# Kernel optimization log

Hardware: AMD Instinct MI355X
Metric: run time of the kernel (lower is better)

The kernel has to match this reference:

```python
import jax, jax.numpy as jnp
import numpy as np

DIM = 512
EXPAND = 2
D_INNER = DIM * EXPAND            # 1024
HEADDIM = DIM * EXPAND // 8       # 128
NHEADS = D_INNER // HEADDIM       # 8
D_STATE = 128
D_CONV = 4
CONV_DIM = D_INNER + 2 * D_STATE  # 1280 (x, B, C channels)
D_IN_PROJ = 2 * D_INNER + 2 * D_STATE + NHEADS  # 2312
BSZ = 4
IMG = (16, 16, 16)                # 4096 tokens


def setup_inputs() -> dict:
    key = jax.random.key(0)
    ks = jax.random.split(key, 8)
    x = jax.random.normal(ks[0], (BSZ, DIM, *IMG), jnp.float32)
    in_proj_w = jax.random.normal(ks[1], (D_IN_PROJ, DIM), jnp.float32) * (DIM ** -0.5)
    conv_w = jax.random.normal(ks[2], (CONV_DIM, D_CONV), jnp.float32) * 0.3
    conv_b = jax.random.normal(ks[3], (CONV_DIM,), jnp.float32) * 0.1
    dt_bias = jax.random.normal(ks[4], (NHEADS,), jnp.float32) * 0.5
    A_log = jnp.log(jnp.arange(1, NHEADS + 1, dtype=jnp.float32))
    D_param = jnp.ones((NHEADS,), jnp.float32) + 0.1 * jax.random.normal(ks[5], (NHEADS,), jnp.float32)
    norm_w = jnp.ones((D_INNER,), jnp.float32)
    out_proj_w = jax.random.normal(ks[6], (DIM, D_INNER), jnp.float32) * (D_INNER ** -0.5)
    return dict(x=x, in_proj_w=in_proj_w, conv_w=conv_w, conv_b=conv_b,
                dt_bias=dt_bias, A_log=A_log, D_param=D_param,
                norm_w=norm_w, out_proj_w=out_proj_w)


def reference(x, in_proj_w, conv_w, conv_b, dt_bias, A_log, D_param, norm_w, out_proj_w):
    Bsz, C = x.shape[:2]
    img_dims = x.shape[2:]
    u = x.reshape(Bsz, C, -1).transpose(0, 2, 1)          # [b, L, d_model]
    L = u.shape[1]

    zxbcdt = jnp.einsum('bld,ed->ble', u, in_proj_w)      # [b, L, 2312]
    z = zxbcdt[..., :D_INNER]                             # gate
    xBC = zxbcdt[..., D_INNER:D_INNER + CONV_DIM]
    dt = zxbcdt[..., D_INNER + CONV_DIM:]                 # [b, L, h]
    dt = jax.nn.softplus(dt + dt_bias)

    # causal depthwise conv1d (kernel 4) + SiLU
    xp = jnp.pad(xBC, ((0, 0), (D_CONV - 1, 0), (0, 0)))
    conv = conv_b + sum(xp[:, k:k + L, :] * conv_w[:, k] for k in range(D_CONV))
    xBC = jax.nn.silu(conv)

    xs = xBC[..., :D_INNER].reshape(Bsz, L, NHEADS, HEADDIM)   # [b, L, h, p]
    Bmat = xBC[..., D_INNER:D_INNER + D_STATE]                 # [b, L, n] (ngroups=1)
    Cmat = xBC[..., D_INNER + D_STATE:]                        # [b, L, n]

    A = -jnp.exp(A_log)                                        # [h]
    dA = jnp.exp(dt * A)                                       # [b, L, h]

    def step(state, inp):
        # state: [b, h, p, n]
        x_t, B_t, C_t, dA_t, dt_t = inp
        state = state * dA_t[:, :, None, None] + \
                jnp.einsum('bhp,bn->bhpn', dt_t[:, :, None] * x_t, B_t)
        y_t = jnp.einsum('bhpn,bn->bhp', state, C_t)
        return state, y_t

    init = jnp.zeros((Bsz, NHEADS, HEADDIM, D_STATE), x.dtype)
    inputs = (xs.transpose(1, 0, 2, 3), Bmat.transpose(1, 0, 2),
              Cmat.transpose(1, 0, 2), dA.transpose(1, 0, 2), dt.transpose(1, 0, 2))
    _, ys = jax.lax.scan(step, init, inputs)                   # ys: [L, b, h, p]

    y = ys.transpose(1, 0, 2, 3) + D_param[None, None, :, None] * xs
    y = y.reshape(Bsz, L, D_INNER)

    # gated RMSNorm (norm_before_gate=False): rmsnorm(y * silu(z)) * w
    y = y * jax.nn.silu(z)
    y = y * jax.lax.rsqrt(jnp.mean(y * y, axis=-1, keepdims=True) + 1e-5) * norm_w

    out = jnp.einsum('ble,de->bld', y, out_proj_w)             # [b, L, d_model]
    out = out.transpose(0, 2, 1).reshape(Bsz, C, *img_dims)
    return out + x
```

## Files before the change

kernel.cpp:

```cpp
#include <hip/hip_runtime.h>
#include <cstdint>
#include <cstddef>

#define DIMC     512
#define D_INNER  1024
#define HEADDIM  128
#define NHEADS   8
#define D_STATE  128
#define CONV_DIM 1280
#define D_IN_PROJ 2312
#define NPAD     2432
#define BSZ      4
#define LSEQ     4096
#define BLTOT    (BSZ*LSEQ)
#define QC       64
#define NCH      (LSEQ/QC)

typedef short bf16x8 __attribute__((ext_vector_type(8)));
typedef float f32x4  __attribute__((ext_vector_type(4)));
typedef _Float16 f16x8 __attribute__((ext_vector_type(8)));
typedef _Float16 f16x4 __attribute__((ext_vector_type(4)));

__device__ inline ushort f2bf(float f) {
    uint32_t u = __float_as_uint(f);
    uint32_t r = (u + 0x7FFFu + ((u >> 16) & 1u)) >> 16;
    return (ushort)r;
}

__device__ __forceinline__ void gload_lds16(const void* g, void* l) {
    __builtin_amdgcn_global_load_lds(
        (const __attribute__((address_space(1))) void*)g,
        (__attribute__((address_space(3))) void*)l,
        16, 0, 0);
}

__global__ __launch_bounds__(256) void k0_prep(
    const float* __restrict__ x, ushort* __restrict__ xT,
    const float* __restrict__ Win, ushort* __restrict__ Wb,
    const float* __restrict__ Wout, ushort* __restrict__ WoutB)
{
    const int bx = blockIdx.x;
    if (bx < 8192) {
        __shared__ float t[32][33];
        const int lt = bx & 127, dt = (bx >> 7) & 15, b = bx >> 11;
        const int r = threadIdx.x >> 5, c = threadIdx.x & 31;
        #pragma unroll
        for (int i = 0; i < 4; ++i) {
            int d = dt * 32 + r + i * 8;
            t[r + i * 8][c] = x[((size_t)(b * DIMC + d) << 12) + lt * 32 + c];
        }
        __syncthreads();
        #pragma unroll
        for (int i = 0; i < 4; ++i) {
            int l = lt * 32 + r + i * 8;
            xT[((size_t)(b * LSEQ + l)) * DIMC + dt * 32 + c] = f2bf(t[c][r + i * 8]);
        }
    } else if (bx < 9408) {
        int i4 = ((bx - 8192) * 256 + threadIdx.x) * 4;
        int e = i4 >> 9;
        ushort4 o;
        if (e < D_IN_PROJ) {
            float4 v = *(const float4*)(Win + (size_t)e * DIMC + (i4 & 511));
            o.x = f2bf(v.x); o.y = f2bf(v.y); o.z = f2bf(v.z); o.w = f2bf(v.w);
        } else { o.x = o.y = o.z = o.w = 0; }
        *(ushort4*)(Wb + i4) = o;
    } else {
        int i4 = ((bx - 9408) * 256 + threadIdx.x) * 4;
        float4 v = *(const float4*)(Wout + i4);
        ushort4 o;
        o.x = f2bf(v.x); o.y = f2bf(v.y); o.z = f2bf(v.z); o.w = f2bf(v.w);
        *(ushort4*)(WoutB + i4) = o;
    }
}

__global__ __launch_bounds__(256) void k1_mfma(
    const ushort* __restrict__ A, const ushort* __restrict__ B,
    _Float16* __restrict__ zh, _Float16* __restrict__ xbcPre, float* __restrict__ dtb)
{
    __shared__ ushort sA[128 * 32];
    __shared__ ushort sB[128 * 32];
    const int tid = threadIdx.x;
    const int lane = tid & 63;
    const int wv = tid >> 6;
    const int wm = (wv & 1) * 64, wn = (wv >> 1) * 64;
    const int m0 = blockIdx.x * 128;
    const int n0 = blockIdx.y * 128;

    f32x4 acc[4][4];
    #pragma unroll
    for (int i = 0; i < 4; ++i)
        #pragma unroll
        for (int j = 0; j < 4; ++j) acc[i][j] = (f32x4){0.f, 0.f, 0.f, 0.f};

    const int r0 = tid >> 2, c0 = tid & 3, k80 = c0 ^ ((r0 >> 1) & 3);
    const int s1_ = tid + 256;
    const int r1 = s1_ >> 2, c1 = s1_ & 3, k81 = c1 ^ ((r1 >> 1) & 3);
    const int quad = lane >> 4, col = lane & 15;
    ushort* lA0 = sA + (size_t)(wv * 64) * 8;
    ushort* lA1 = sA + (size_t)(256 + wv * 64) * 8;
    ushort* lB0 = sB + (size_t)(wv * 64) * 8;
    ushort* lB1 = sB + (size_t)(256 + wv * 64) * 8;

    for (int kb = 0; kb < DIMC; kb += 32) {
        gload_lds16(A + (size_t)(m0 + r0) * DIMC + kb + k80 * 8, lA0);
        gload_lds16(A + (size_t)(m0 + r1) * DIMC + kb + k81 * 8, lA1);
        gload_lds16(B + (size_t)(n0 + r0) * DIMC + kb + k80 * 8, lB0);
        gload_lds16(B + (size_t)(n0 + r1) * DIMC + kb + k81 * 8, lB1);
        __syncthreads();
        bf16x8 af[4], bf_[4];
        #pragma unroll
        for (int mi = 0; mi < 4; ++mi) {
            int m = wm + mi * 16 + col;
            int ch = quad ^ ((m >> 1) & 3);
            af[mi] = *(const bf16x8*)&sA[m * 32 + ch * 8];
        }
        #pragma unroll
        for (int ni = 0; ni < 4; ++ni) {
            int n = wn + ni * 16 + col;
            int ch = quad ^ ((n >> 1) & 3);
            bf_[ni] = *(const bf16x8*)&sB[n * 32 + ch * 8];
        }
        #pragma unroll
        for (int mi = 0; mi < 4; ++mi)
            #pragma unroll
            for (int ni = 0; ni < 4; ++ni)
                acc[mi][ni] = __builtin_amdgcn_mfma_f32_16x16x32_bf16(af[mi], bf_[ni], acc[mi][ni], 0, 0, 0);
        __syncthreads();
    }

    #pragma unroll
    for (int mi = 0; mi < 4; ++mi) {
        #pragma unroll
        for (int ni = 0; ni < 4; ++ni) {
            int e = n0 + wn + ni * 16 + col;
            #pragma unroll
            for (int reg = 0; reg < 4; ++reg) {
                int m = m0 + wm + mi * 16 + quad * 4 + reg;
                float v = acc[mi][ni][reg];
                if (e < D_INNER)                  zh[(size_t)m * D_INNER + e] = (_Float16)v;
                else if (e < D_INNER + CONV_DIM)  xbcPre[(size_t)m * CONV_DIM + (e - D_INNER)] = (_Float16)v;
                else if (e < D_IN_PROJ)           dtb[(size_t)m * NHEADS + (e - (D_INNER + CONV_DIM))] = v;
            }
        }
    }
}

__global__ __launch_bounds__(256) void k2_dt(
    const float* __restrict__ dtb, const float* __restrict__ dt_bias,
    const float* __restrict__ A_log, float* __restrict__ dtp, float* __restrict__ ldA)
{
    int idx = blockIdx.x * 256 + threadIdx.x;
    if (idx >= BLTOT * NHEADS) return;
    int h = idx & 7;
    float v = dtb[idx] + dt_bias[h];
    float sp = (v > 20.f) ? v : log1pf(expf(v));
    dtp[idx] = sp;
    ldA[idx] = sp * (-expf(A_log[h]));
}

__global__ __launch_bounds__(256) void k3_conv(
    const _Float16* __restrict__ xbcPre, const float* __restrict__ cw,
    const float* __restrict__ cb, _Float16* __restrict__ xsT,
    _Float16* __restrict__ bcNat, _Float16* __restrict__ BT)
{
    __shared__ _Float16 tT[32][36];
    const int tid = threadIdx.x;
    const int tq = tid >> 3, cg = tid & 7;
    const float4* cw4 = (const float4*)cw;
    if (blockIdx.x < 16384) {
        const int bx = blockIdx.x;
        const int ct = bx & 31, tt = (bx >> 5) & 127, b = bx >> 12;
        const int t0 = tt * 32, c0 = ct * 32;
        const int t = t0 + tq;
        const int c = c0 + cg * 4;
        const int m = b * LSEQ + t;

        float4 b4 = *(const float4*)&cb[c];
        float4 w0 = cw4[c], w1 = cw4[c + 1], w2 = cw4[c + 2], w3 = cw4[c + 3];
        float acc[4] = {b4.x, b4.y, b4.z, b4.w};
        {
            f16x4 xv = *(const f16x4*)&xbcPre[(size_t)m * CONV_DIM + c];
            acc[0] = fmaf((float)xv[0], w0.w, acc[0]);
            acc[1] = fmaf((float)xv[1], w1.w, acc[1]);
            acc[2] = fmaf((float)xv[2], w2.w, acc[2]);
            acc[3] = fmaf((float)xv[3], w3.w, acc[3]);
        }
        if (t >= 1) {
            f16x4 xv = *(const f16x4*)&xbcPre[(size_t)(m - 1) * CONV_DIM + c];
            acc[0] = fmaf((float)xv[0], w0.z, acc[0]);
            acc[1] = fmaf((float)xv[1], w1.z, acc[1]);
            acc[2] = fmaf((float)xv[2], w2.z, acc[2]);
            acc[3] = fmaf((float)xv[3], w3.z, acc[3]);
        }
        if (t >= 2) {
            f16x4 xv = *(const f16x4*)&xbcPre[(size_t)(m - 2) * CONV_DIM + c];
            acc[0] = fmaf((float)xv[0], w0.y, acc[0]);
            acc[1] = fmaf((float)xv[1], w1.y, acc[1]);
            acc[2] = fmaf((float)xv[2], w2.y, acc[2]);
            acc[3] = fmaf((float)xv[3], w3.y, acc[3]);
        }
        if (t >= 3) {
            f16x4 xv = *(const f16x4*)&xbcPre[(size_t)(m - 3) * CONV_DIM + c];
            acc[0] = fmaf((float)xv[0], w0.x, acc[0]);
            acc[1] = fmaf((float)xv[1], w1.x, acc[1]);
            acc[2] = fmaf((float)xv[2], w2.x, acc[2]);
            acc[3] = fmaf((float)xv[3], w3.x, acc[3]);
        }
        #pragma unroll
        for (int i = 0; i < 4; ++i) {
            float s = acc[i] / (1.f + expf(-acc[i]));
            tT[cg * 4 + i][tq] = (_Float16)s;
        }
        __syncthreads();
        const int r = tid >> 3, g = tid & 7;
        f16x4 o = *(const f16x4*)&tT[r][g * 4];
        *(f16x4*)&xsT[((size_t)b * D_INNER + c0 + r) * LSEQ + t0 + g * 4] = o;
    } else {
        const int bx = blockIdx.x - 16384;
        const int ct = bx & 7, tt = (bx >> 3) & 127, b = bx >> 10;
        const int t0 = tt * 32, c0 = ct * 32;
        const int t = t0 + tq;
        const int ca = 1024 + c0 + cg * 4;
        const int m = b * LSEQ + t;

        float4 b4 = *(const float4*)&cb[ca];
        float4 w0 = cw4[ca], w1 = cw4[ca + 1], w2 = cw4[ca + 2], w3 = cw4[ca + 3];
        float acc[4] = {b4.x, b4.y, b4.z, b4.w};
        {
            f16x4 xv = *(const f16x4*)&xbcPre[(size_t)m * CONV_DIM + ca];
            acc[0] = fmaf((float)xv[0], w0.w, acc[0]);
            acc[1] = fmaf((float)xv[1], w1.w, acc[1]);
            acc[2] = fmaf((float)xv[2], w2.w, acc[2]);
            acc[3] = fmaf((float)xv[3], w3.w, acc[3]);
        }
        if (t >= 1) {
            f16x4 xv = *(const f16x4*)&xbcPre[(size_t)(m - 1) * CONV_DIM + ca];
            acc[0] = fmaf((float)xv[0], w0.z, acc[0]);
            acc[1] = fmaf((float)xv[1], w1.z, acc[1]);
            acc[2] = fmaf((float)xv[2], w2.z, acc[2]);
            acc[3] = fmaf((float)xv[3], w3.z, acc[3]);
        }
        if (t >= 2) {
            f16x4 xv = *(const f16x4*)&xbcPre[(size_t)(m - 2) * CONV_DIM + ca];
            acc[0] = fmaf((float)xv[0], w0.y, acc[0]);
            acc[1] = fmaf((float)xv[1], w1.y, acc[1]);
            acc[2] = fmaf((float)xv[2], w2.y, acc[2]);
            acc[3] = fmaf((float)xv[3], w3.y, acc[3]);
        }
        if (t >= 3) {
            f16x4 xv = *(const f16x4*)&xbcPre[(size_t)(m - 3) * CONV_DIM + ca];
            acc[0] = fmaf((float)xv[0], w0.x, acc[0]);
            acc[1] = fmaf((float)xv[1], w1.x, acc[1]);
            acc[2] = fmaf((float)xv[2], w2.x, acc[2]);
            acc[3] = fmaf((float)xv[3], w3.x, acc[3]);
        }
        f16x4 nat;
        #pragma unroll
        for (int i = 0; i < 4; ++i) {
            float s = acc[i] / (1.f + expf(-acc[i]));
            nat[i] = (_Float16)s;
            tT[cg * 4 + i][tq] = nat[i];
        }
        *(f16x4*)&bcNat[(size_t)m * 256 + c0 + cg * 4] = nat;
        if (ct < 4) {
            __syncthreads();
            const int r = tid >> 3, g = tid & 7;
            f16x4 o = *(const f16x4*)&tT[r][g * 4];
            *(f16x4*)&BT[((size_t)b * D_STATE + c0 + r) * LSEQ + t0 + g * 4] = o;
        }
    }
}

__global__ __launch_bounds__(256) void k4aA(
    const _Float16* __restrict__ xsT, const _Float16* __restrict__ BT,
    const float* __restrict__ dtp, const float* __restrict__ ldA,
    _Float16* __restrict__ ST, float* __restrict__ Pbuf)
{
    __shared__ char smem[128 * 72 * 2 * 2 + 512];
    _Float16* sXTs = (_Float16*)smem;
    _Float16* sBT  = sXTs + 128 * 72;
    float* sW = (float*)(sBT + 128 * 72);
    _Float16* sOut = sXTs;

    const int tid = threadIdx.x;
    const int lane = tid & 63;
    const int wv = tid >> 6;
    const int quad = lane >> 4, l15 = lane & 15;
    const int c = blockIdx.x & 63;
    const int h = (blockIdx.x >> 6) & 7;
    const int b = blockIdx.x >> 9;
    const int bh = b * NHEADS + h;
    const size_t mbase = (size_t)b * LSEQ + c * QC;

    if (tid < 64) {
        size_t gi = (mbase + tid) * NHEADS + h;
        float ld = ldA[gi];
        float dtv = dtp[gi];
        float cum = ld;
        #pragma unroll
        for (int off = 1; off < 64; off <<= 1) {
            float v = __shfl_up(cum, off);
            if (tid >= off) cum += v;
        }
        float cum63 = __shfl(cum, 63);
        sW[tid] = expf(cum63 - cum) * dtv;
        if (tid == 63) Pbuf[bh * NCH + c] = expf(cum63);
    }
    __syncthreads();

    #pragma unroll
    for (int k = 0; k < 4; ++k) {
        int idx = k * 256 + tid;
        int row = idx >> 3, g = idx & 7;
        int t0 = g * 8;
        f16x8 hv = *(const f16x8*)&xsT[((size_t)b * D_INNER + h * HEADDIM + row) * LSEQ + c * QC + t0];
        f16x8 sv;
        #pragma unroll
        for (int j = 0; j < 8; ++j) sv[j] = (_Float16)((float)hv[j] * sW[t0 + j]);
        *(f16x8*)&sXTs[row * 72 + t0] = sv;
        int4 bv = *(const int4*)&BT[((size_t)b * D_STATE + row) * LSEQ + c * QC + t0];
        *(int4*)&sBT[row * 72 + t0] = bv;
    }
    __syncthreads();

    f32x4 acc[2][8];
    #pragma unroll
    for (int i = 0; i < 2; ++i)
        #pragma unroll
        for (int j = 0; j < 8; ++j) acc[i][j] = (f32x4){0.f, 0.f, 0.f, 0.f};

    #pragma unroll
    for (int kk = 0; kk < 2; ++kk) {
        f16x8 af[2];
        #pragma unroll
        for (int mi = 0; mi < 2; ++mi)
            af[mi] = *(const f16x8*)&sXTs[(wv * 32 + mi * 16 + l15) * 72 + kk * 32 + quad * 8];
        #pragma unroll
        for (int ni = 0; ni < 8; ++ni) {
            f16x8 bf_ = *(const f16x8*)&sBT[(ni * 16 + l15) * 72 + kk * 32 + quad * 8];
            #pragma unroll
            for (int mi = 0; mi < 2; ++mi)
                acc[mi][ni] = __builtin_amdgcn_mfma_f32_16x16x32_f16(af[mi], bf_, acc[mi][ni], 0, 0, 0);
        }
    }
    __syncthreads();
    #pragma unroll
    for (int mi = 0; mi < 2; ++mi)
        #pragma unroll
        for (int ni = 0; ni < 8; ++ni)
            #pragma unroll
            for (int reg = 0; reg < 4; ++reg) {
                int p = wv * 32 + mi * 16 + quad * 4 + reg;
                int n = ni * 16 + l15;
                sOut[p * 136 + n] = (_Float16)acc[mi][ni][reg];
            }
    __syncthreads();
    _Float16* stg = ST + ((size_t)bh * NCH + c) * (HEADDIM * D_STATE);
    #pragma unroll
    for (int k = 0; k < 8; ++k) {
        int idx = k * 256 + tid;
        int row = idx >> 4, g = idx & 15;
        int4 v = *(const int4*)&sOut[row * 136 + g * 8];
        *(int4*)&stg[row * 128 + g * 8] = v;
    }
}

__global__ __launch_bounds__(256) void k4bB(_Float16* __restrict__ ST, const float* __restrict__ Pbuf)
{
    __shared__ float sp_[NCH];
    const int bh = blockIdx.x >> 4;
    const int seg = blockIdx.x & 15;
    const int tid = threadIdx.x;
    if (tid < NCH) sp_[tid] = Pbuf[bh * NCH + tid];
    __syncthreads();
    const int e = seg * 1024 + tid * 4;
    float r0 = 0.f, r1 = 0.f, r2 = 0.f, r3 = 0.f;
    for (int c = 0; c < NCH; ++c) {
        _Float16* ptr = ST + ((size_t)bh * NCH + c) * (HEADDIM * D_STATE) + e;
        f16x4 v = *(const f16x4*)ptr;
        float f0 = (float)v[0], f1 = (float)v[1], f2 = (float)v[2], f3 = (float)v[3];
        f16x4 o; o[0] = (_Float16)r0; o[1] = (_Float16)r1; o[2] = (_Float16)r2; o[3] = (_Float16)r3;
        *(f16x4*)ptr = o;
        float P = sp_[c];
        r0 = fmaf(r0, P, f0); r1 = fmaf(r1, P, f1);
        r2 = fmaf(r2, P, f2); r3 = fmaf(r3, P, f3);
    }
}

__global__ __launch_bounds__(256) void k4cC(
    const _Float16* __restrict__ bcNat, const _Float16* __restrict__ xsT,
    const _Float16* __restrict__ sinit, const float* __restrict__ dtp,
    const float* __restrict__ ldA, const float* __restrict__ Dp,
    _Float16* __restrict__ yB)
{
    __shared__ char smem[(64*136 + 64*136 + 128*72 + 4*16*72) * 2 + 640];
    _Float16* sC  = (_Float16*)smem;
    _Float16* sB  = sC + 64 * 136;
    _Float16* sXT = sB + 64 * 136;
    _Float16* sM  = sXT + 128 * 72;
    float* scum = (float*)(sM + 4 * 16 * 72);
    float* sdt  = scum + 64;
    _Float16* sIni = sB;
    _Float16* sY  = sC;

    const int tid = threadIdx.x;
    const int lane = tid & 63;
    const int wv = tid >> 6;
    const int quad = lane >> 4, l15 = lane & 15;
    const int c = blockIdx.x & 63;
    const int h = (blockIdx.x >> 6) & 7;
    const int b = blockIdx.x >> 9;
    const int bh = b * NHEADS + h;
    const size_t mbase = (size_t)b * LSEQ + c * QC;
    const float Dh = Dp[h];

    if (tid < 64) {
        size_t gi = (mbase + tid) * NHEADS + h;
        float ld = ldA[gi];
        float dtv = dtp[gi];
        float cum = ld;
        #pragma unroll
        for (int off = 1; off < 64; off <<= 1) {
            float v = __shfl_up(cum, off);
            if (tid >= off) cum += v;
        }
        scum[tid] = cum;
        sdt[tid] = dtv;
    }
    #pragma unroll
    for (int k = 0; k < 4; ++k) {
        int idx = k * 256 + tid;
        int t = idx >> 4, g = idx & 15;
        const _Float16* row = bcNat + (mbase + t) * 256;
        *(int4*)&sB[t * 136 + g * 8] = *(const int4*)&row[g * 8];
        *(int4*)&sC[t * 136 + g * 8] = *(const int4*)&row[128 + g * 8];
        int idx2 = k * 256 + tid;
        int p = idx2 >> 3, g2 = idx2 & 7;
        *(int4*)&sXT[p * 72 + g2 * 8] =
            *(const int4*)&xsT[((size_t)b * D_INNER + h * HEADDIM + p) * LSEQ + c * QC + g2 * 8];
    }
    __syncthreads();

    f32x4 g[4];
    #pragma unroll
    for (int j = 0; j < 4; ++j) g[j] = (f32x4){0.f, 0.f, 0.f, 0.f};
    #pragma unroll
    for (int kk = 0; kk < 4; ++kk) {
        f16x8 af = *(const f16x8*)&sC[(wv * 16 + l15) * 136 + kk * 32 + quad * 8];
        #pragma unroll
        for (int tt = 0; tt < 4; ++tt) {
            f16x8 bf_ = *(const f16x8*)&sB[(tt * 16 + l15) * 136 + kk * 32 + quad * 8];
            g[tt] = __builtin_amdgcn_mfma_f32_16x16x32_f16(af, bf_, g[tt], 0, 0, 0);
        }
    }
    _Float16* sMw = sM + wv * 16 * 72;
    #pragma unroll
    for (int tt = 0; tt < 4; ++tt) {
        int tau = tt * 16 + l15;
        #pragma unroll
        for (int reg = 0; reg < 4; ++reg) {
            int trow = quad * 4 + reg;
            int tglob = wv * 16 + trow;
            float mval;
            if (tau > tglob) mval = 0.f;
            else if (tau == tglob) mval = g[tt][reg] * sdt[tau] + Dh;
            else mval = g[tt][reg] * expf(scum[tglob] - scum[tau]) * sdt[tau];
            sMw[trow * 72 + tau] = (_Float16)mval;
        }
    }
    asm volatile("s_waitcnt lgkmcnt(0)" ::: "memory");

    f32x4 y[8];
    #pragma unroll
    for (int j = 0; j < 8; ++j) y[j] = (f32x4){0.f, 0.f, 0.f, 0.f};
    #pragma unroll
    for (int kk = 0; kk < 2; ++kk) {
        f16x8 af = *(const f16x8*)&sMw[l15 * 72 + kk * 32 + quad * 8];
        #pragma unroll
        for (int pi = 0; pi < 8; ++pi) {
            f16x8 bf_ = *(const f16x8*)&sXT[(pi * 16 + l15) * 72 + kk * 32 + quad * 8];
            y[pi] = __builtin_amdgcn_mfma_f32_16x16x32_f16(af, bf_, y[pi], 0, 0, 0);
        }
    }
    __syncthreads();
    {
        const _Float16* sg = sinit + ((size_t)bh * NCH + c) * (HEADDIM * D_STATE);
        #pragma unroll
        for (int k = 0; k < 8; ++k) {
            int idx = k * 256 + tid;
            int p = idx >> 4, gg = idx & 15;
            *(int4*)&sIni[p * 136 + gg * 8] = *(const int4*)&sg[p * 128 + gg * 8];
        }
    }
    __syncthreads();
    {
        float ea = expf(scum[wv * 16 + l15]);
        #pragma unroll
        for (int kk = 0; kk < 4; ++kk) {
            f16x8 cf = *(const f16x8*)&sC[(wv * 16 + l15) * 136 + kk * 32 + quad * 8];
            f16x8 af;
            #pragma unroll
            for (int j = 0; j < 8; ++j) af[j] = (_Float16)((float)cf[j] * ea);
            #pragma unroll
            for (int pi = 0; pi < 8; ++pi) {
                f16x8 bf_ = *(const f16x8*)&sIni[(pi * 16 + l15) * 136 + kk * 32 + quad * 8];
                y[pi] = __builtin_amdgcn_mfma_f32_16x16x32_f16(af, bf_, y[pi], 0, 0, 0);
            }
        }
    }
    __syncthreads();
    #pragma unroll
    for (int pi = 0; pi < 8; ++pi)
        #pragma unroll
        for (int reg = 0; reg < 4; ++reg) {
            int trow = wv * 16 + quad * 4 + reg;
            int p = pi * 16 + l15;
            sY[trow * 136 + p] = (_Float16)y[pi][reg];
        }
    __syncthreads();
    #pragma unroll
    for (int k = 0; k < 4; ++k) {
        int idx = k * 256 + tid;
        int t = idx >> 4, gg = idx & 15;
        int4 v = *(const int4*)&sY[t * 136 + gg * 8];
        *(int4*)&yB[(mbase + t) * D_INNER + h * HEADDIM + gg * 8] = v;
    }
}

__global__ __launch_bounds__(256) void k5_norm(
    const _Float16* __restrict__ yB, const _Float16* __restrict__ zh,
    const float* __restrict__ nw, ushort* __restrict__ ybB)
{
    const int m = blockIdx.x;
    const int tid = threadIdx.x;
    const size_t off = (size_t)m * D_INNER + tid * 4;
    f16x4 yv = *(const f16x4*)&yB[off];
    f16x4 zv = *(const f16x4*)&zh[off];
    float4 gv;
    {
        float z0 = (float)zv[0], z1 = (float)zv[1], z2 = (float)zv[2], z3 = (float)zv[3];
        gv.x = (float)yv[0] * (z0 / (1.f + expf(-z0)));
        gv.y = (float)yv[1] * (z1 / (1.f + expf(-z1)));
        gv.z = (float)yv[2] * (z2 / (1.f + expf(-z2)));
        gv.w = (float)yv[3] * (z3 / (1.f + expf(-z3)));
    }
    float ss = gv.x*gv.x + gv.y*gv.y + gv.z*gv.z + gv.w*gv.w;
    #pragma unroll
    for (int mask = 1; mask <= 32; mask <<= 1) ss += __shfl_xor(ss, mask);
    __shared__ float red[4];
    if ((tid & 63) == 0) red[tid >> 6] = ss;
    __syncthreads();
    float tot = red[0] + red[1] + red[2] + red[3];
    float scale = rsqrtf(tot * (1.f / 1024.f) + 1e-5f);
    float4 w4 = *(const float4*)(nw + tid * 4);
    ushort4 ob;
    ob.x = f2bf(gv.x * scale * w4.x);
    ob.y = f2bf(gv.y * scale * w4.y);
    ob.z = f2bf(gv.z * scale * w4.z);
    ob.w = f2bf(gv.w * scale * w4.w);
    *(ushort4*)(ybB + off) = ob;
}

__global__ __launch_bounds__(256) void k6_mfma(
    const ushort* __restrict__ A, const ushort* __restrict__ B,
    const float* __restrict__ x, float* __restrict__ out)
{
    __shared__ ushort sA[128 * 32];
    __shared__ ushort sB[128 * 32];
    const int tid = threadIdx.x;
    const int lane = tid & 63;
    const int wv = tid >> 6;
    const int wm = (wv & 1) * 64, wn = (wv >> 1) * 64;
    const int m0 = blockIdx.x * 128;
    const int n0 = blockIdx.y * 128;

    f32x4 acc[4][4];
    #pragma unroll
    for (int i = 0; i < 4; ++i)
        #pragma unroll
        for (int j = 0; j < 4; ++j) acc[i][j] = (f32x4){0.f, 0.f, 0.f, 0.f};

    const int r0 = tid >> 2, c0 = tid & 3, k80 = c0 ^ ((r0 >> 1) & 3);
    const int s1_ = tid + 256;
    const int r1 = s1_ >> 2, c1 = s1_ & 3, k81 = c1 ^ ((r1 >> 1) & 3);
    const int quad = lane >> 4, col = lane & 15;
    ushort* lA0 = sA + (size_t)(wv * 64) * 8;
    ushort* lA1 = sA + (size_t)(256 + wv * 64) * 8;
    ushort* lB0 = sB + (size_t)(wv * 64) * 8;
    ushort* lB1 = sB + (size_t)(256 + wv * 64) * 8;

    for (int kb = 0; kb < D_INNER; kb += 32) {
        gload_lds16(A + (size_t)(m0 + r0) * D_INNER + kb + k80 * 8, lA0);
        gload_lds16(A + (size_t)(m0 + r1) * D_INNER + kb + k81 * 8, lA1);
        gload_lds16(B + (size_t)(n0 + r0) * D_INNER + kb + k80 * 8, lB0);
        gload_lds16(B + (size_t)(n0 + r1) * D_INNER + kb + k81 * 8, lB1);
        __syncthreads();
        bf16x8 af[4], bf_[4];
        #pragma unroll
        for (int mi = 0; mi < 4; ++mi) {
            int m = wm + mi * 16 + col;
            int ch = quad ^ ((m >> 1) & 3);
            af[mi] = *(const bf16x8*)&sA[m * 32 + ch * 8];
        }
        #pragma unroll
        for (int ni = 0; ni < 4; ++ni) {
            int n = wn + ni * 16 + col;
            int ch = quad ^ ((n >> 1) & 3);
            bf_[ni] = *(const bf16x8*)&sB[n * 32 + ch * 8];
        }
        #pragma unroll
        for (int mi = 0; mi < 4; ++mi)
            #pragma unroll
            for (int ni = 0; ni < 4; ++ni)
                acc[mi][ni] = __builtin_amdgcn_mfma_f32_16x16x32_bf16(af[mi], bf_[ni], acc[mi][ni], 0, 0, 0);
        __syncthreads();
    }

    #pragma unroll
    for (int mi = 0; mi < 4; ++mi) {
        #pragma unroll
        for (int ni = 0; ni < 4; ++ni) {
            int mm = n0 + wn + ni * 16 + col;
            int b = mm >> 12, l = mm & 4095;
            #pragma unroll
            for (int reg = 0; reg < 4; ++reg) {
                int d = m0 + wm + mi * 16 + quad * 4 + reg;
                size_t o = ((size_t)(b * DIMC + d) << 12) + l;
                out[o] = acc[mi][ni][reg] + x[o];
            }
        }
    }
}

extern "C" void kernel_launch(void* const* d_in, const int* in_sizes, int n_in,
                              void* d_out, int out_size, void* d_ws, size_t ws_size,
                              hipStream_t stream) {
    const float* x          = (const float*)d_in[0];
    const float* in_proj_w  = (const float*)d_in[1];
    const float* conv_w     = (const float*)d_in[2];
    const float* conv_b     = (const float*)d_in[3];
    const float* dt_bias    = (const float*)d_in[4];
    const float* A_log      = (const float*)d_in[5];
    const float* D_param    = (const float*)d_in[6];
    const float* norm_w     = (const float*)d_in[7];
    const float* out_proj_w = (const float*)d_in[8];
    float* out = (float*)d_out;

    float* ws = (float*)d_ws;
    float* zbuf = ws;
    _Float16* zh = (_Float16*)zbuf;
    float* regB = zbuf + (size_t)16777216;
    _Float16* xbcPre = (_Float16*)regB;
    _Float16* yB     = (_Float16*)regB;
    float* dtb  = regB + (size_t)10485760;
    float* dtp  = dtb + 131072;
    float* ldA  = dtp + 131072;
    float* Pbuf = ldA + 131072;
    float* regD = Pbuf + 2048;
    ushort* xT_k1 = (ushort*)regD;
    ushort* Wb    = xT_k1 + (size_t)BLTOT * DIMC;
    _Float16* ST  = (_Float16*)regD;
    float* regE = regD + (size_t)16777216;
    _Float16* xsT   = (_Float16*)regE;
    _Float16* BT    = xsT + (size_t)BSZ * D_INNER * LSEQ;
    _Float16* bcNat = BT + (size_t)BSZ * D_STATE * LSEQ;
    ushort* woutB   = (ushort*)(bcNat + (size_t)BLTOT * 256);

    k0_prep<<<dim3(9920), dim3(256), 0, stream>>>(x, xT_k1, in_proj_w, Wb, out_proj_w, woutB);
    k1_mfma<<<dim3(128, 19), dim3(256), 0, stream>>>(xT_k1, Wb, zh, xbcPre, dtb);
    k2_dt<<<dim3(512), dim3(256), 0, stream>>>(dtb, dt_bias, A_log, dtp, ldA);
    k3_conv<<<dim3(20480), dim3(256), 0, stream>>>(xbcPre, conv_w, conv_b, xsT, bcNat, BT);
    k4aA<<<dim3(2048), dim3(256), 0, stream>>>(xsT, BT, dtp, ldA, ST, Pbuf);
    k4bB<<<dim3(512), dim3(256), 0, stream>>>(ST, Pbuf);
    k4cC<<<dim3(2048), dim3(256), 0, stream>>>(bcNat, xsT, ST, dtp, ldA, D_param, yB);
    k5_norm<<<dim3(BLTOT), dim3(256), 0, stream>>>(yB, zh, norm_w, (ushort*)yB);
    k6_mfma<<<dim3(4, 128), dim3(256), 0, stream>>>(woutB, (ushort*)yB, x, out);
}
```

Measured before the change: 359.4 us.

## Fuse dt softplus into scan kernels and prefetch chunk initial state early

Removes the separate k2_dt kernel and recomputes softplus(dt+bias) and dt*A inside k4aA and k4cC, where the values are consumed. This saves one launch and a write/read round trip of two small buffers, at the cost of redundant transcendental work per block. k4cC also issues the global loads of the chunk's initial state into registers at kernel start, overlapping their latency with the earlier MFMA work, which raises register pressure.

After: 377.3 us. +5.0%, slower.

```diff
diff --git a/kernel.cpp b/kernel.cpp
--- a/kernel.cpp
+++ b/kernel.cpp
@@ -32,6 +32,13 @@
         (const __attribute__((address_space(1))) void*)g,
         (__attribute__((address_space(3))) void*)l,
         16, 0, 0);
+}
+
+__device__ __forceinline__ void dt_transform(float raw, float bias, float alog,
+                                             float& sp, float& ld) {
+    float v0 = raw + bias;
+    sp = (v0 > 20.f) ? v0 : log1pf(expf(v0));
+    ld = sp * (-expf(alog));
 }
 
 __global__ __launch_bounds__(256) void k0_prep(
@@ -145,19 +152,6 @@
     }
 }
 
-__global__ __launch_bounds__(256) void k2_dt(
-    const float* __restrict__ dtb, const float* __restrict__ dt_bias,
-    const float* __restrict__ A_log, float* __restrict__ dtp, float* __restrict__ ldA)
-{
-    int idx = blockIdx.x * 256 + threadIdx.x;
-    if (idx >= BLTOT * NHEADS) return;
-    int h = idx & 7;
-    float v = dtb[idx] + dt_bias[h];
-    float sp = (v > 20.f) ? v : log1pf(expf(v));
-    dtp[idx] = sp;
-    ldA[idx] = sp * (-expf(A_log[h]));
-}
-
 __global__ __launch_bounds__(256) void k3_conv(
     const _Float16* __restrict__ xbcPre, const float* __restrict__ cw,
     const float* __restrict__ cb, _Float16* __restrict__ xsT,
@@ -273,7 +267,8 @@
 
 __global__ __launch_bounds__(256) void k4aA(
     const _Float16* __restrict__ xsT, const _Float16* __restrict__ BT,
-    const float* __restrict__ dtp, const float* __restrict__ ldA,
+    const float* __restrict__ dtb, const float* __restrict__ dt_bias,
+    const float* __restrict__ A_log,
     _Float16* __restrict__ ST, float* __restrict__ Pbuf)
 {
     __shared__ char smem[128 * 72 * 2 * 2 + 512];
@@ -294,8 +289,8 @@
 
     if (tid < 64) {
         size_t gi = (mbase + tid) * NHEADS + h;
-        float ld = ldA[gi];
-        float dtv = dtp[gi];
+        float sp, ld;
+        dt_transform(dtb[gi], dt_bias[h], A_log[h], sp, ld);
         float cum = ld;
         #pragma unroll
         for (int off = 1; off < 64; off <<= 1) {
@@ -303,7 +298,7 @@
             if (tid >= off) cum += v;
         }
         float cum63 = __shfl(cum, 63);
-        sW[tid] = expf(cum63 - cum) * dtv;
+        sW[tid] = expf(cum63 - cum) * sp;
         if (tid == 63) Pbuf[bh * NCH + c] = expf(cum63);
     }
     __syncthreads();
@@ -389,9 +384,9 @@
 
 __global__ __launch_bounds__(256) void k4cC(
     const _Float16* __restrict__ bcNat, const _Float16* __restrict__ xsT,
-    const _Float16* __restrict__ sinit, const float* __restrict__ dtp,
-    const float* __restrict__ ldA, const float* __restrict__ Dp,
-    _Float16* __restrict__ yB)
+    const _Float16* __restrict__ sinit, const float* __restrict__ dtb,
+    const float* __restrict__ dt_bias, const float* __restrict__ A_log,
+    const float* __restrict__ Dp, _Float16* __restrict__ yB)
 {
     __shared__ char smem[(64*136 + 64*136 + 128*72 + 4*16*72) * 2 + 640];
     _Float16* sC  = (_Float16*)smem;
@@ -414,10 +409,21 @@
     const size_t mbase = (size_t)b * LSEQ + c * QC;
     const float Dh = Dp[h];
 
+    int4 pre[8];
+    {
+        const _Float16* sg = sinit + ((size_t)bh * NCH + c) * (HEADDIM * D_STATE);
+        #pragma unroll
+        for (int k = 0; k < 8; ++k) {
+            int idx = k * 256 + tid;
+            int p = idx >> 4, gg = idx & 15;
+            pre[k] = *(const int4*)&sg[p * 128 + gg * 8];
+        }
+    }
+
     if (tid < 64) {
         size_t gi = (mbase + tid) * NHEADS + h;
-        float ld = ldA[gi];
-        float dtv = dtp[gi];
+        float sp, ld;
+        dt_transform(dtb[gi], dt_bias[h], A_log[h], sp, ld);
         float cum = ld;
         #pragma unroll
         for (int off = 1; off < 64; off <<= 1) {
@@ -425,7 +431,7 @@
             if (tid >= off) cum += v;
         }
         scum[tid] = cum;
-        sdt[tid] = dtv;
+        sdt[tid] = sp;
     }
     #pragma unroll
     for (int k = 0; k < 4; ++k) {
@@ -484,12 +490,11 @@
     }
     __syncthreads();
     {
-        const _Float16* sg = sinit + ((size_t)bh * NCH + c) * (HEADDIM * D_STATE);
         #pragma unroll
         for (int k = 0; k < 8; ++k) {
             int idx = k * 256 + tid;
             int p = idx >> 4, gg = idx & 15;
-            *(int4*)&sIni[p * 136 + gg * 8] = *(const int4*)&sg[p * 128 + gg * 8];
+            *(int4*)&sIni[p * 136 + gg * 8] = pre[k];
         }
     }
     __syncthreads();
@@ -653,9 +658,7 @@
     _Float16* xbcPre = (_Float16*)regB;
     _Float16* yB     = (_Float16*)regB;
     float* dtb  = regB + (size_t)10485760;
-    float* dtp  = dtb + 131072;
-    float* ldA  = dtp + 131072;
-    float* Pbuf = ldA + 131072;
+    float* Pbuf = dtb + 131072 * 3;
     float* regD = Pbuf + 2048;
     ushort* xT_k1 = (ushort*)regD;
     ushort* Wb    = xT_k1 + (size_t)BLTOT * DIMC;
@@ -668,11 +671,10 @@
 
     k0_prep<<<dim3(9920), dim3(256), 0, stream>>>(x, xT_k1, in_proj_w, Wb, out_proj_w, woutB);
     k1_mfma<<<dim3(128, 19), dim3(256), 0, stream>>>(xT_k1, Wb, zh, xbcPre, dtb);
-    k2_dt<<<dim3(512), dim3(256), 0, stream>>>(dtb, dt_bias, A_log, dtp, ldA);
     k3_conv<<<dim3(20480), dim3(256), 0, stream>>>(xbcPre, conv_w, conv_b, xsT, bcNat, BT);
-    k4aA<<<dim3(2048), dim3(256), 0, stream>>>(xsT, BT, dtp, ldA, ST, Pbuf);
+    k4aA<<<dim3(2048), dim3(256), 0, stream>>>(xsT, BT, dtb, dt_bias, A_log, ST, Pbuf);
     k4bB<<<dim3(512), dim3(256), 0, stream>>>(ST, Pbuf);
-    k4cC<<<dim3(2048), dim3(256), 0, stream>>>(bcNat, xsT, ST, dtp, ldA, D_param, yB);
+    k4cC<<<dim3(2048), dim3(256), 0, stream>>>(bcNat, xsT, ST, dtb, dt_bias, A_log, D_param, yB);
     k5_norm<<<dim3(BLTOT), dim3(256), 0, stream>>>(yB, zh, norm_w, (ushort*)yB);
     k6_mfma<<<dim3(4, 128), dim3(256), 0, stream>>>(woutB, (ushort*)yB, x, out);
 }
```
